# Kernel optimization log

Hardware: AMD Instinct MI355X
Metric: run time of the kernel (lower is better)

## Reference

```python
import jax, jax.numpy as jnp
import numpy as np

B, S, DIM, H, FFN = 2, 2048, 1024, 16, 4096
HD = DIM // H
THETA = 10000.0
EPS = 1e-5


def setup_inputs() -> dict:
    key = jax.random.key(0)
    ks = jax.random.split(key, 12)
    s = 0.02
    return {
        "x": jax.random.normal(ks[0], (B, S, DIM), jnp.float32),
        "padding_mask": jnp.zeros((B, S), jnp.bool_),
        "qkv_w": jax.random.normal(ks[1], (DIM, 3 * DIM), jnp.float32) * s,
        "qkv_b": jnp.zeros((3 * DIM,), jnp.float32),
        "out_w": jax.random.normal(ks[2], (DIM, DIM), jnp.float32) * s,
        "out_b": jnp.zeros((DIM,), jnp.float32),
        "ln1_g": jnp.ones((DIM,), jnp.float32),
        "ln1_b": jnp.zeros((DIM,), jnp.float32),
        "ln2_g": jnp.ones((DIM,), jnp.float32),
        "ln2_b": jnp.zeros((DIM,), jnp.float32),
        "w1": jax.random.normal(ks[3], (DIM, FFN), jnp.float32) * s,
        "b1": jnp.zeros((FFN,), jnp.float32),
        "w2": jax.random.normal(ks[4], (FFN, DIM), jnp.float32) * s,
        "b2": jnp.zeros((DIM,), jnp.float32),
    }


def _layer_norm(x, g, b):
    mu = jnp.mean(x, axis=-1, keepdims=True)
    var = jnp.mean(jnp.square(x - mu), axis=-1, keepdims=True)
    return (x - mu) * jax.lax.rsqrt(var + EPS) * g + b


def _rotate_half(x):
    x1, x2 = jnp.split(x, 2, axis=-1)
    return jnp.concatenate([-x2, x1], axis=-1)


def reference(x, padding_mask, qkv_w, qkv_b, out_w, out_b,
              ln1_g, ln1_b, ln2_g, ln2_b, w1, b1, w2, b2):
    b, s, _ = x.shape
    residual = x
    h = _layer_norm(x, ln1_g, ln1_b)
    qkv = h @ qkv_w + qkv_b  # [b, s, 3*dim]
    q, k, v = jnp.split(qkv, 3, axis=-1)
    # [b, heads, s, head_dim]
    q = q.reshape(b, s, H, HD).transpose(0, 2, 1, 3)
    k = k.reshape(b, s, H, HD).transpose(0, 2, 1, 3)
    v = v.reshape(b, s, H, HD).transpose(0, 2, 1, 3)

    # rotary embeddings
    pos = jnp.arange(s, dtype=jnp.float32)
    inv_freq = 1.0 / (THETA ** (jnp.arange(0, HD, 2, dtype=jnp.float32) / HD))
    freqs = pos[:, None] * inv_freq[None, :]          # [s, hd/2]
    emb = jnp.concatenate([freqs, freqs], axis=-1)    # [s, hd]
    sin = jnp.sin(emb)[None, None, :, :]
    cos = jnp.cos(emb)[None, None, :, :]
    q = q * cos + _rotate_half(q) * sin
    k = k * cos + _rotate_half(k) * sin

    scale = HD ** (-0.5)
    scores = jnp.einsum('bhqd,bhkd->bhqk', q, k) * scale
    neg = jnp.finfo(scores.dtype).min
    scores = jnp.where(padding_mask[:, None, None, :], neg, scores)
    probs = jax.nn.softmax(scores, axis=-1)
    ctx = jnp.einsum('bhqk,bhkd->bhqd', probs, v)
    ctx = ctx.transpose(0, 2, 1, 3).reshape(b, s, DIM)
    x = residual + (ctx @ out_w + out_b)

    residual = x
    h = _layer_norm(x, ln2_g, ln2_b)
    h = jax.nn.gelu(h @ w1 + b1, approximate=False) @ w2 + b2
    return residual + h
```

## Files before the change

kernel.cpp:

```cpp
#include <hip/hip_runtime.h>
#include <hip/hip_bf16.h>
#include <math.h>

typedef __hip_bfloat16 bf16;
typedef __attribute__((ext_vector_type(8))) short short8;
typedef __attribute__((ext_vector_type(4))) float floatx4;

constexpr int BB   = 2;
constexpr int SS   = 2048;
constexpr int DIMc = 1024;
constexpr int Hc   = 16;
constexpr int HDc  = 64;
constexpr int FFNc = 4096;
constexpr int TOK  = BB * SS;
constexpr float EPSc = 1e-5f;

typedef __attribute__((address_space(1))) void gvoid;
typedef __attribute__((address_space(3))) void lvoid;
__device__ __forceinline__ void lds16(const void* g, void* l) {
    __builtin_amdgcn_global_load_lds((gvoid*)g, (lvoid*)l, 16, 0, 0);
}
__device__ __forceinline__ float fexp2(float x) { return __builtin_amdgcn_exp2f(x); }

__global__ __launch_bounds__(256) void ln_kernel(const float* __restrict__ x,
                                                 const float* __restrict__ g,
                                                 const float* __restrict__ b,
                                                 bf16* __restrict__ out) {
    int t = blockIdx.x;
    int tid = threadIdx.x;
    float4 v = ((const float4*)(x + (size_t)t * DIMc))[tid];
    float s  = v.x + v.y + v.z + v.w;
    float sq = v.x*v.x + v.y*v.y + v.z*v.z + v.w*v.w;
    for (int off = 1; off < 64; off <<= 1) {
        s  += __shfl_xor(s,  off, 64);
        sq += __shfl_xor(sq, off, 64);
    }
    __shared__ float ss[4], ssq[4];
    int wave = tid >> 6;
    if ((tid & 63) == 0) { ss[wave] = s; ssq[wave] = sq; }
    __syncthreads();
    s  = ss[0] + ss[1] + ss[2] + ss[3];
    sq = ssq[0] + ssq[1] + ssq[2] + ssq[3];
    float mu  = s * (1.0f / DIMc);
    float var = sq * (1.0f / DIMc) - mu * mu;
    float inv = rsqrtf(var + EPSc);
    float4 gg = ((const float4*)g)[tid];
    float4 bb = ((const float4*)b)[tid];
    size_t base = (size_t)t * DIMc + tid * 4;
    out[base + 0] = __float2bfloat16((v.x - mu) * inv * gg.x + bb.x);
    out[base + 1] = __float2bfloat16((v.y - mu) * inv * gg.y + bb.y);
    out[base + 2] = __float2bfloat16((v.z - mu) * inv * gg.z + bb.z);
    out[base + 3] = __float2bfloat16((v.w - mu) * inv * gg.w + bb.w);
}

__global__ __launch_bounds__(256) void reduce_ln_kernel(const float* __restrict__ P,
                                                        const float* __restrict__ x,
                                                        const float* __restrict__ bias,
                                                        const float* __restrict__ g,
                                                        const float* __restrict__ b,
                                                        float* __restrict__ out,
                                                        bf16* __restrict__ hout) {
    int t = blockIdx.x;
    int tid = threadIdx.x;
    size_t off = (size_t)t * DIMc / 4 + tid;
    float4 v  = ((const float4*)x)[off];
    float4 p0 = ((const float4*)P)[off];
    float4 p1 = ((const float4*)P)[off + (size_t)TOK * DIMc / 4];
    float4 bv = ((const float4*)bias)[tid];
    v.x += p0.x + p1.x + bv.x;
    v.y += p0.y + p1.y + bv.y;
    v.z += p0.z + p1.z + bv.z;
    v.w += p0.w + p1.w + bv.w;
    ((float4*)out)[off] = v;

    float s  = v.x + v.y + v.z + v.w;
    float sq = v.x*v.x + v.y*v.y + v.z*v.z + v.w*v.w;
    for (int o = 1; o < 64; o <<= 1) {
        s  += __shfl_xor(s,  o, 64);
        sq += __shfl_xor(sq, o, 64);
    }
    __shared__ float ss[4], ssq[4];
    int wave = tid >> 6;
    if ((tid & 63) == 0) { ss[wave] = s; ssq[wave] = sq; }
    __syncthreads();
    s  = ss[0] + ss[1] + ss[2] + ss[3];
    sq = ssq[0] + ssq[1] + ssq[2] + ssq[3];
    float mu  = s * (1.0f / DIMc);
    float var = sq * (1.0f / DIMc) - mu * mu;
    float inv = rsqrtf(var + EPSc);
    float4 gg = ((const float4*)g)[tid];
    float4 bb = ((const float4*)b)[tid];
    size_t base = (size_t)t * DIMc + tid * 4;
    hout[base + 0] = __float2bfloat16((v.x - mu) * inv * gg.x + bb.x);
    hout[base + 1] = __float2bfloat16((v.y - mu) * inv * gg.y + bb.y);
    hout[base + 2] = __float2bfloat16((v.z - mu) * inv * gg.z + bb.z);
    hout[base + 3] = __float2bfloat16((v.w - mu) * inv * gg.w + bb.w);
}

__global__ __launch_bounds__(256) void reduce_add_kernel(const float* __restrict__ P,
                                                         const float* __restrict__ bias,
                                                         float* __restrict__ out) {
    size_t f = (size_t)blockIdx.x * 256 + threadIdx.x;
    float4 v  = ((float4*)out)[f];
    float4 p0 = ((const float4*)P)[f];
    float4 p1 = ((const float4*)P)[f + (size_t)TOK * DIMc / 4];
    float4 bv = ((const float4*)bias)[f & (DIMc / 4 - 1)];
    v.x += p0.x + p1.x + bv.x;
    v.y += p0.y + p1.y + bv.y;
    v.z += p0.z + p1.z + bv.z;
    v.w += p0.w + p1.w + bv.w;
    ((float4*)out)[f] = v;
}

__global__ __launch_bounds__(256) void transpose_bf16(const float* __restrict__ in,
                                                      bf16* __restrict__ out,
                                                      int K, int N) {
    __shared__ float t[32][33];
    int k0 = blockIdx.y * 32, n0 = blockIdx.x * 32;
    int x = threadIdx.x & 31;
    int y = threadIdx.x >> 5;
#pragma unroll
    for (int i = 0; i < 4; ++i) {
        int k = y + i * 8;
        t[k][x] = in[(size_t)(k0 + k) * N + n0 + x];
    }
    __syncthreads();
#pragma unroll
    for (int i = 0; i < 4; ++i) {
        int n = y + i * 8;
        out[(size_t)(n0 + n) * K + k0 + x] = __float2bfloat16(t[x][n]);
    }
}

__global__ __launch_bounds__(256) void transpose_v(const bf16* __restrict__ qkv,
                                                   bf16* __restrict__ vT) {
    __shared__ short t[64][72];
    const int s0 = blockIdx.x * 64, h = blockIdx.y, b = blockIdx.z;
    const int tid = threadIdx.x;
    const short* qs = (const short*)qkv;
#pragma unroll
    for (int it = 0; it < 2; ++it) {
        int idx = it * 256 + tid;
        int r = idx >> 3, c = (idx & 7) * 8;
        *(short8*)&t[r][c] = *(const short8*)(qs + (size_t)(b * SS + s0 + r) * 3072
                                              + 2048 + h * 64 + c);
    }
    __syncthreads();
#pragma unroll
    for (int it = 0; it < 2; ++it) {
        int idx = it * 256 + tid;
        int d = idx >> 3, cs = (idx & 7) * 8;
        short8 v;
#pragma unroll
        for (int j = 0; j < 8; ++j) v[j] = t[cs + j][d];
        *(short8*)((short*)vT + ((size_t)(b * Hc + h) * 64 + d) * SS + s0 + cs) = v;
    }
}

template <int ACT, bool ROPE>
__global__ __launch_bounds__(256) void gemm_bt(const bf16* __restrict__ A,
                                               const bf16* __restrict__ Bt,
                                               const float* __restrict__ bias,
                                               bf16* __restrict__ Cout,
                                               int M, int N, int K) {
    constexpr int BK = 64;
    __shared__ bf16 As[2][128 * 32];
    __shared__ bf16 Bs[2][128 * 32];
    const int tid = threadIdx.x;
    const int wave = tid >> 6, lane = tid & 63;
    const int lane15 = lane & 15, lgrp = lane >> 4;
    const int wm = (wave >> 1) * 64, wn = (wave & 1) * 64;
    const int row0 = blockIdx.y * 128, col0 = blockIdx.x * 128;

    floatx4 acc[4][4] = {};

    const int srow = wave * 16 + (lane >> 2);
    const int scol = (lane & 3) * 8;
    const bf16* ga = A  + (size_t)(row0 + srow) * K + scol;
    const bf16* gb = Bt + (size_t)(col0 + srow) * K + scol;

    for (int k0 = 0; k0 < K; k0 += BK) {
        __syncthreads();
#pragma unroll
        for (int p = 0; p < 4; ++p) {
            const size_t go = (size_t)((p & 1) * 64) * K + k0 + (p >> 1) * 32;
            lds16(ga + go, &As[p >> 1][(p & 1) * 2048 + wave * 512]);
            lds16(gb + go, &Bs[p >> 1][(p & 1) * 2048 + wave * 512]);
        }
        __syncthreads();
#pragma unroll
        for (int s = 0; s < 2; ++s) {
            short8 af[4], bfr[4];
#pragma unroll
            for (int i = 0; i < 4; ++i)
                af[i] = *(const short8*)(&As[s][(wm + i * 16 + lane15) * 32 + lgrp * 8]);
#pragma unroll
            for (int j = 0; j < 4; ++j)
                bfr[j] = *(const short8*)(&Bs[s][(wn + j * 16 + lane15) * 32 + lgrp * 8]);
#pragma unroll
            for (int i = 0; i < 4; ++i)
#pragma unroll
                for (int j = 0; j < 4; ++j)
                    acc[i][j] = __builtin_amdgcn_mfma_f32_16x16x32_bf16(af[i], bfr[j], acc[i][j], 0, 0, 0);
        }
    }

    const bool doRope = ROPE && (col0 < 2048);
    float invf0 = 0.f, invf1 = 0.f;
    if (ROPE) {
        invf0 = fexp2(-0.4152410118609203f * (float)lane15);
        invf1 = fexp2(-0.4152410118609203f * (float)(16 + lane15));
    }
    float bv[4];
#pragma unroll
    for (int j = 0; j < 4; ++j) bv[j] = bias[col0 + wn + j * 16 + lane15];

#pragma unroll
    for (int i = 0; i < 4; ++i) {
#pragma unroll
        for (int r = 0; r < 4; ++r) {
            int row = row0 + wm + i * 16 + lgrp * 4 + r;
            float v[4];
#pragma unroll
            for (int j = 0; j < 4; ++j) v[j] = acc[i][j][r] + bv[j];
            if (doRope) {
                float pos = (float)(row & (SS - 1));
                float s0, c0, s1, c1;
                __sincosf(pos * invf0, &s0, &c0);
                __sincosf(pos * invf1, &s1, &c1);
                float t0 = v[0] * c0 - v[2] * s0;
                float t1 = v[1] * c1 - v[3] * s1;
                float t2 = v[2] * c0 + v[0] * s0;
                float t3 = v[3] * c1 + v[1] * s1;
                v[0] = t0; v[1] = t1; v[2] = t2; v[3] = t3;
            }
#pragma unroll
            for (int j = 0; j < 4; ++j) {
                float o = v[j];
                if (ACT == 1) o = 0.5f * o * (1.0f + erff(o * 0.70710678118654752f));
                Cout[(size_t)row * N + col0 + wn + j * 16 + lane15] = __float2bfloat16(o);
            }
        }
    }
}

__global__ __launch_bounds__(256) void gemm_bt_splitk(const bf16* __restrict__ A,
                                                      const bf16* __restrict__ Bt,
                                                      float* __restrict__ P,
                                                      int M, int N, int K, int KCH) {
    constexpr int BK = 64;
    __shared__ bf16 As[2][128 * 32];
    __shared__ bf16 Bs[2][128 * 32];
    const int tid = threadIdx.x;
    const int wave = tid >> 6, lane = tid & 63;
    const int lane15 = lane & 15, lgrp = lane >> 4;
    const int wm = (wave >> 1) * 64, wn = (wave & 1) * 64;
    const int row0 = blockIdx.y * 128, col0 = blockIdx.x * 128;
    const int kbase = blockIdx.z * KCH;
    float* Cp = P + (size_t)blockIdx.z * M * N;

    floatx4 acc[4][4] = {};

    const int srow = wave * 16 + (lane >> 2);
    const int scol = (lane & 3) * 8;
    const bf16* ga = A  + (size_t)(row0 + srow) * K + scol;
    const bf16* gb = Bt + (size_t)(col0 + srow) * K + scol;

    for (int k0 = kbase; k0 < kbase + KCH; k0 += BK) {
        __syncthreads();
#pragma unroll
        for (int p = 0; p < 4; ++p) {
            const size_t go = (size_t)((p & 1) * 64) * K + k0 + (p >> 1) * 32;
            lds16(ga + go, &As[p >> 1][(p & 1) * 2048 + wave * 512]);
            lds16(gb + go, &Bs[p >> 1][(p & 1) * 2048 + wave * 512]);
        }
        __syncthreads();
#pragma unroll
        for (int s = 0; s < 2; ++s) {
            short8 af[4], bfr[4];
#pragma unroll
            for (int i = 0; i < 4; ++i)
                af[i] = *(const short8*)(&As[s][(wm + i * 16 + lane15) * 32 + lgrp * 8]);
#pragma unroll
            for (int j = 0; j < 4; ++j)
                bfr[j] = *(const short8*)(&Bs[s][(wn + j * 16 + lane15) * 32 + lgrp * 8]);
#pragma unroll
            for (int i = 0; i < 4; ++i)
#pragma unroll
                for (int j = 0; j < 4; ++j)
                    acc[i][j] = __builtin_amdgcn_mfma_f32_16x16x32_bf16(af[i], bfr[j], acc[i][j], 0, 0, 0);
        }
    }

#pragma unroll
    for (int i = 0; i < 4; ++i)
#pragma unroll
        for (int j = 0; j < 4; ++j) {
            int col = col0 + wn + j * 16 + lane15;
#pragma unroll
            for (int r = 0; r < 4; ++r) {
                int row = row0 + wm + i * 16 + lgrp * 4 + r;
                Cp[(size_t)row * N + col] = acc[i][j][r];
            }
        }
}

__global__ __launch_bounds__(256) void attn_mfma(const bf16* __restrict__ qkv,
                                                 const bf16* __restrict__ vT,
                                                 const unsigned char* __restrict__ mask,
                                                 float* __restrict__ Op,
                                                 float* __restrict__ Lp) {
    __shared__ short Klds[2][64][32];
    __shared__ short Vlds[2][64][32];
    __shared__ short Ps[4][32][72];
    __shared__ float mkf[64];

    const int h = blockIdx.y;
    const int b = blockIdx.z >> 1, kc = blockIdx.z & 1;
    const int q0 = blockIdx.x * 128;
    const int tid = threadIdx.x;
    const int wave = tid >> 6, lane = tid & 63;
    const int lane15 = lane & 15, lgrp = lane >> 4;
    const short* qs = (const short*)qkv;
    const short* vs = (const short*)vT + (size_t)(b * Hc + h) * 64 * SS;

    short* qstage = &Ps[wave][0][0];
#pragma unroll
    for (int i = 0; i < 4; ++i) {
        int idx = i * 64 + lane;
        int g = idx & 3, row = (idx >> 2) & 15, s = (idx >> 6) & 1, mi = idx >> 7;
        const short* gq = qs + (size_t)(b * SS + q0 + wave * 32 + mi * 16 + row) * 3072
                             + h * 64 + s * 32 + g * 8;
        lds16(gq, qstage + idx * 8);
    }
    __syncthreads();
    short8 aQ[2][2];
#pragma unroll
    for (int mi = 0; mi < 2; ++mi)
#pragma unroll
        for (int s = 0; s < 2; ++s)
            aQ[mi][s] = *(const short8*)(qstage + ((mi * 2 + s) * 16 + lane15) * 32 + lgrp * 8);

    const short8 bOnes = (short8)(short)0x3F80;
    floatx4 O[2][4] = {};
    floatx4 Lacc[2] = {};
    const float cscale = 0.18033688011112042f;

    for (int t = 0; t < 16; ++t) {
        const int k0 = kc * 1024 + t * 64;
        __syncthreads();
#pragma unroll
        for (int i = 0; i < 2; ++i) {
            int idx = wave * 128 + i * 64 + lane;
            int g = idx & 3, row = (idx >> 2) & 63, s = idx >> 8;
            const short* gk = qs + (size_t)(b * SS + k0 + row) * 3072 + 1024
                                 + h * 64 + s * 32 + g * 8;
            lds16(gk, &Klds[0][0][0] + idx * 8);
        }
#pragma unroll
        for (int i = 0; i < 2; ++i) {
            int idx = wave * 128 + i * 64 + lane;
            int g = idx & 3, drow = (idx >> 2) & 63, s = idx >> 8;
            const short* gv = vs + (size_t)drow * SS + k0 + s * 32 + g * 8;
            lds16(gv, &Vlds[0][0][0] + idx * 8);
        }
        if (tid < 16) {
            const unsigned char* mp = mask + b * SS + k0 + tid * 4;
#pragma unroll
            for (int j = 0; j < 4; ++j) mkf[tid * 4 + j] = mp[j] ? -1e30f : 0.0f;
        }
        __syncthreads();

        short8 bK[4][2];
#pragma unroll
        for (int j = 0; j < 4; ++j)
#pragma unroll
            for (int s = 0; s < 2; ++s)
                bK[j][s] = *(const short8*)&Klds[s][j * 16 + lane15][lgrp * 8];
        floatx4 Sf[2][4] = {};
#pragma unroll
        for (int mi = 0; mi < 2; ++mi)
#pragma unroll
            for (int j = 0; j < 4; ++j)
#pragma unroll
                for (int s = 0; s < 2; ++s)
                    Sf[mi][j] = __builtin_amdgcn_mfma_f32_16x16x32_bf16(aQ[mi][s], bK[j][s], Sf[mi][j], 0, 0, 0);

        float mkv[4];
#pragma unroll
        for (int j = 0; j < 4; ++j) mkv[j] = mkf[j * 16 + lane15];

#pragma unroll
        for (int mi = 0; mi < 2; ++mi)
#pragma unroll
            for (int r = 0; r < 4; ++r)
#pragma unroll
                for (int j = 0; j < 4; ++j) {
                    float p = fexp2(Sf[mi][j][r] * cscale + mkv[j]);
                    bf16 tt = __float2bfloat16(p);
                    Ps[wave][mi * 16 + lgrp * 4 + r][lane15 + 16 * j] = *(short*)&tt;
                }

        short8 aP[2][2], bV[4][2];
#pragma unroll
        for (int mi = 0; mi < 2; ++mi)
#pragma unroll
            for (int s = 0; s < 2; ++s)
                aP[mi][s] = *(const short8*)&Ps[wave][mi * 16 + lane15][s * 32 + lgrp * 8];
#pragma unroll
        for (int jd = 0; jd < 4; ++jd)
#pragma unroll
            for (int s = 0; s < 2; ++s)
                bV[jd][s] = *(const short8*)&Vlds[s][jd * 16 + lane15][lgrp * 8];
#pragma unroll
        for (int mi = 0; mi < 2; ++mi) {
#pragma unroll
            for (int jd = 0; jd < 4; ++jd)
#pragma unroll
                for (int s = 0; s < 2; ++s)
                    O[mi][jd] = __builtin_amdgcn_mfma_f32_16x16x32_bf16(aP[mi][s], bV[jd][s], O[mi][jd], 0, 0, 0);
#pragma unroll
            for (int s = 0; s < 2; ++s)
                Lacc[mi] = __builtin_amdgcn_mfma_f32_16x16x32_bf16(aP[mi][s], bOnes, Lacc[mi], 0, 0, 0);
        }
    }

    float* myOp = Op + (size_t)kc * TOK * DIMc;
#pragma unroll
    for (int mi = 0; mi < 2; ++mi)
#pragma unroll
        for (int r = 0; r < 4; ++r) {
            int q = q0 + wave * 32 + mi * 16 + lgrp * 4 + r;
            size_t rowoff = (size_t)(b * SS + q) * DIMc + h * 64 + lane15;
#pragma unroll
            for (int jd = 0; jd < 4; ++jd)
                myOp[rowoff + jd * 16] = O[mi][jd][r];
            if (lane15 == 0)
                Lp[((size_t)kc * TOK + b * SS + q) * Hc + h] = Lacc[mi][r];
        }
}

__global__ __launch_bounds__(256) void attn_combine(const float* __restrict__ Op,
                                                    const float* __restrict__ Lp,
                                                    bf16* __restrict__ ctx) {
    int t = blockIdx.x;
    int tid = threadIdx.x;
    int h = tid >> 4;
    size_t f = (size_t)t * (DIMc / 4) + tid;
    float4 p0 = ((const float4*)Op)[f];
    float4 p1 = ((const float4*)Op)[f + (size_t)TOK * DIMc / 4];
    float inv = 1.0f / (Lp[(size_t)t * Hc + h] + Lp[((size_t)TOK + t) * Hc + h]);
    size_t base = (size_t)t * DIMc + tid * 4;
    ctx[base + 0] = __float2bfloat16((p0.x + p1.x) * inv);
    ctx[base + 1] = __float2bfloat16((p0.y + p1.y) * inv);
    ctx[base + 2] = __float2bfloat16((p0.z + p1.z) * inv);
    ctx[base + 3] = __float2bfloat16((p0.w + p1.w) * inv);
}

extern "C" void kernel_launch(void* const* d_in, const int* in_sizes, int n_in,
                              void* d_out, int out_size, void* d_ws, size_t ws_size,
                              hipStream_t stream) {
    const float* x      = (const float*)d_in[0];
    const unsigned char* pmask = (const unsigned char*)d_in[1];
    const float* qkv_w  = (const float*)d_in[2];
    const float* qkv_b  = (const float*)d_in[3];
    const float* out_w  = (const float*)d_in[4];
    const float* out_b  = (const float*)d_in[5];
    const float* ln1_g  = (const float*)d_in[6];
    const float* ln1_b  = (const float*)d_in[7];
    const float* ln2_g  = (const float*)d_in[8];
    const float* ln2_b  = (const float*)d_in[9];
    const float* w1     = (const float*)d_in[10];
    const float* b1     = (const float*)d_in[11];
    const float* w2     = (const float*)d_in[12];
    const float* b2     = (const float*)d_in[13];
    float* out = (float*)d_out;

    char* ws = (char*)d_ws;
    bf16* wqkv_t = (bf16*)ws;                      ws += (size_t)3072 * 1024 * 2;
    bf16* wout_t = (bf16*)ws;                      ws += (size_t)1024 * 1024 * 2;
    bf16* w1_t   = (bf16*)ws;                      ws += (size_t)4096 * 1024 * 2;
    bf16* w2_t   = (bf16*)ws;                      ws += (size_t)1024 * 4096 * 2;
    bf16* h_bf   = (bf16*)ws;                      ws += (size_t)TOK * DIMc * 2;
    bf16* qkv_bf = (bf16*)ws;                      ws += (size_t)TOK * 3 * DIMc * 2;
    bf16* ctx_bf = (bf16*)ws;                      ws += (size_t)TOK * DIMc * 2;
    float* partial = (float*)ws;                   ws += (size_t)2 * TOK * DIMc * 4;
    float* Lp      = (float*)ws;                   ws += (size_t)2 * TOK * Hc * 4;
    bf16* ffn1_bf = qkv_bf;
    bf16* vT      = h_bf;

    transpose_bf16<<<dim3(3072 / 32, 1024 / 32), 256, 0, stream>>>(qkv_w, wqkv_t, 1024, 3072);
    transpose_bf16<<<dim3(1024 / 32, 1024 / 32), 256, 0, stream>>>(out_w, wout_t, 1024, 1024);
    transpose_bf16<<<dim3(4096 / 32, 1024 / 32), 256, 0, stream>>>(w1,    w1_t,   1024, 4096);
    transpose_bf16<<<dim3(1024 / 32, 4096 / 32), 256, 0, stream>>>(w2,    w2_t,   4096, 1024);

    ln_kernel<<<TOK, 256, 0, stream>>>(x, ln1_g, ln1_b, h_bf);
    gemm_bt<0, true><<<dim3(3072 / 128, TOK / 128), 256, 0, stream>>>(
        h_bf, wqkv_t, qkv_b, qkv_bf, TOK, 3 * DIMc, DIMc);
    transpose_v<<<dim3(SS / 64, Hc, BB), 256, 0, stream>>>(qkv_bf, vT);
    attn_mfma<<<dim3(SS / 128, Hc, BB * 2), 256, 0, stream>>>(qkv_bf, vT, pmask, partial, Lp);
    attn_combine<<<TOK, 256, 0, stream>>>(partial, Lp, ctx_bf);

    gemm_bt_splitk<<<dim3(1024 / 128, TOK / 128, 2), 256, 0, stream>>>(
        ctx_bf, wout_t, partial, TOK, DIMc, DIMc, 512);
    reduce_ln_kernel<<<TOK, 256, 0, stream>>>(partial, x, out_b, ln2_g, ln2_b, out, h_bf);

    gemm_bt<1, false><<<dim3(4096 / 128, TOK / 128), 256, 0, stream>>>(
        h_bf, w1_t, b1, ffn1_bf, TOK, FFNc, DIMc);
    gemm_bt_splitk<<<dim3(1024 / 128, TOK / 128, 2), 256, 0, stream>>>(
        ffn1_bf, w2_t, partial, TOK, DIMc, FFNc, 2048);
    reduce_add_kernel<<<TOK * DIMc / 4 / 256, 256, 0, stream>>>(partial, b2, out);
}
```

Measured before the change: 406.2 us.

## Swizzle LDS tiles in GEMM and attention; remap GEMM blocks across XCDs

Rotates the 16-byte column chunk written into LDS by row index. K/V tiles in attention and A/B tiles in both GEMM kernels are affected, and reads apply the matching inverse rotation, to cut LDS bank conflicts on the MFMA operand loads. The GEMM kernels also remap the linear block id so that blocks landing on the same XCD share nearby row and column tiles, aiming for better L2 reuse. The remap hard-codes the assumption that gridDim.y equals 32 and gridDim.x is even, which holds for these shapes only.

```diff
diff --git a/kernel.cpp b/kernel.cpp
--- a/kernel.cpp
+++ b/kernel.cpp
@@ -157,6 +157,15 @@
     }
 }
 
+__device__ __forceinline__ void xcd_remap(int& bx, int& by) {
+    const int gn = gridDim.x;
+    int lin = blockIdx.y * gn + blockIdx.x;
+    int k8 = lin & 7, idx = lin >> 3;
+    int hn = gn >> 1;
+    by = (k8 >> 1) * 8 + (idx & 7);
+    bx = (k8 & 1) * hn + (idx >> 3);
+}
+
 template <int ACT, bool ROPE>
 __global__ __launch_bounds__(256) void gemm_bt(const bf16* __restrict__ A,
                                                const bf16* __restrict__ Bt,
@@ -170,14 +179,16 @@
     const int wave = tid >> 6, lane = tid & 63;
     const int lane15 = lane & 15, lgrp = lane >> 4;
     const int wm = (wave >> 1) * 64, wn = (wave & 1) * 64;
-    const int row0 = blockIdx.y * 128, col0 = blockIdx.x * 128;
+    int bx, by; xcd_remap(bx, by);
+    const int row0 = by * 128, col0 = bx * 128;
 
     floatx4 acc[4][4] = {};
 
     const int srow = wave * 16 + (lane >> 2);
-    const int scol = (lane & 3) * 8;
+    const int scol = (((lane & 3) + (srow >> 1)) & 3) * 8;
     const bf16* ga = A  + (size_t)(row0 + srow) * K + scol;
     const bf16* gb = Bt + (size_t)(col0 + srow) * K + scol;
+    const int g_l = (lgrp - (lane15 >> 1)) & 3;
 
     for (int k0 = 0; k0 < K; k0 += BK) {
         __syncthreads();
@@ -193,10 +204,10 @@
             short8 af[4], bfr[4];
 #pragma unroll
             for (int i = 0; i < 4; ++i)
-                af[i] = *(const short8*)(&As[s][(wm + i * 16 + lane15) * 32 + lgrp * 8]);
+                af[i] = *(const short8*)(&As[s][(wm + i * 16 + lane15) * 32 + g_l * 8]);
 #pragma unroll
             for (int j = 0; j < 4; ++j)
-                bfr[j] = *(const short8*)(&Bs[s][(wn + j * 16 + lane15) * 32 + lgrp * 8]);
+                bfr[j] = *(const short8*)(&Bs[s][(wn + j * 16 + lane15) * 32 + g_l * 8]);
 #pragma unroll
             for (int i = 0; i < 4; ++i)
 #pragma unroll
@@ -255,16 +266,18 @@
     const int wave = tid >> 6, lane = tid & 63;
     const int lane15 = lane & 15, lgrp = lane >> 4;
     const int wm = (wave >> 1) * 64, wn = (wave & 1) * 64;
-    const int row0 = blockIdx.y * 128, col0 = blockIdx.x * 128;
+    int bx, by; xcd_remap(bx, by);
+    const int row0 = by * 128, col0 = bx * 128;
     const int kbase = blockIdx.z * KCH;
     float* Cp = P + (size_t)blockIdx.z * M * N;
 
     floatx4 acc[4][4] = {};
 
     const int srow = wave * 16 + (lane >> 2);
-    const int scol = (lane & 3) * 8;
+    const int scol = (((lane & 3) + (srow >> 1)) & 3) * 8;
     const bf16* ga = A  + (size_t)(row0 + srow) * K + scol;
     const bf16* gb = Bt + (size_t)(col0 + srow) * K + scol;
+    const int g_l = (lgrp - (lane15 >> 1)) & 3;
 
     for (int k0 = kbase; k0 < kbase + KCH; k0 += BK) {
         __syncthreads();
@@ -280,10 +293,10 @@
             short8 af[4], bfr[4];
 #pragma unroll
             for (int i = 0; i < 4; ++i)
-                af[i] = *(const short8*)(&As[s][(wm + i * 16 + lane15) * 32 + lgrp * 8]);
+                af[i] = *(const short8*)(&As[s][(wm + i * 16 + lane15) * 32 + g_l * 8]);
 #pragma unroll
             for (int j = 0; j < 4; ++j)
-                bfr[j] = *(const short8*)(&Bs[s][(wn + j * 16 + lane15) * 32 + lgrp * 8]);
+                bfr[j] = *(const short8*)(&Bs[s][(wn + j * 16 + lane15) * 32 + g_l * 8]);
 #pragma unroll
             for (int i = 0; i < 4; ++i)
 #pragma unroll
@@ -323,6 +336,7 @@
     const int lane15 = lane & 15, lgrp = lane >> 4;
     const short* qs = (const short*)qkv;
     const short* vs = (const short*)vT + (size_t)(b * Hc + h) * 64 * SS;
+    const int g_l = (lgrp - (lane15 >> 1)) & 3;
 
     short* qstage = &Ps[wave][0][0];
 #pragma unroll
@@ -353,15 +367,17 @@
         for (int i = 0; i < 2; ++i) {
             int idx = wave * 128 + i * 64 + lane;
             int g = idx & 3, row = (idx >> 2) & 63, s = idx >> 8;
+            int gsw = (g + (row >> 1)) & 3;
             const short* gk = qs + (size_t)(b * SS + k0 + row) * 3072 + 1024
-                                 + h * 64 + s * 32 + g * 8;
+                                 + h * 64 + s * 32 + gsw * 8;
             lds16(gk, &Klds[0][0][0] + idx * 8);
         }
 #pragma unroll
         for (int i = 0; i < 2; ++i) {
             int idx = wave * 128 + i * 64 + lane;
             int g = idx & 3, drow = (idx >> 2) & 63, s = idx >> 8;
-            const short* gv = vs + (size_t)drow * SS + k0 + s * 32 + g * 8;
+            int gsw = (g + (drow >> 1)) & 3;
+            const short* gv = vs + (size_t)drow * SS + k0 + s * 32 + gsw * 8;
             lds16(gv, &Vlds[0][0][0] + idx * 8);
         }
         if (tid < 16) {
@@ -376,7 +392,7 @@
         for (int j = 0; j < 4; ++j)
 #pragma unroll
             for (int s = 0; s < 2; ++s)
-                bK[j][s] = *(const short8*)&Klds[s][j * 16 + lane15][lgrp * 8];
+                bK[j][s] = *(const short8*)&Klds[s][j * 16 + lane15][g_l * 8];
         floatx4 Sf[2][4] = {};
 #pragma unroll
         for (int mi = 0; mi < 2; ++mi)
@@ -411,7 +427,7 @@
         for (int jd = 0; jd < 4; ++jd)
 #pragma unroll
             for (int s = 0; s < 2; ++s)
-                bV[jd][s] = *(const short8*)&Vlds[s][jd * 16 + lane15][lgrp * 8];
+                bV[jd][s] = *(const short8*)&Vlds[s][jd * 16 + lane15][g_l * 8];
 #pragma unroll
         for (int mi = 0; mi < 2; ++mi) {
 #pragma unroll
```

Result: faster. 391.5 us (-3.6%).
